# Optimization experiments

Measured on AMD Instinct MI355X. Metric: run time of the kernel, lower is better.

Reference implementation:

```python
import jax, jax.numpy as jnp
import numpy as np

N_NODES = 1_000_000
N_EDGES = 32_000_000
EPS_INIT = 100.0


def setup_inputs() -> dict:
    key = jax.random.key(0)
    ks = jax.random.split(key, 8)
    x = jax.random.normal(ks[0], (N_NODES, 1), dtype=jnp.float32)
    edge_index = jax.random.randint(ks[1], (2, N_EDGES), 0, N_NODES, dtype=jnp.int64)
    # MLP params: Linear(1,20) -> ReLU -> Linear(20,20) -> ReLU -> Linear(20,1)
    w1 = jax.random.normal(ks[2], (1, 20), dtype=jnp.float32) / np.sqrt(1.0)
    b1 = jnp.zeros((20,), dtype=jnp.float32)
    w2 = jax.random.normal(ks[3], (20, 20), dtype=jnp.float32) / np.sqrt(20.0)
    b2 = jnp.zeros((20,), dtype=jnp.float32)
    w3 = jax.random.normal(ks[4], (20, 1), dtype=jnp.float32) / np.sqrt(20.0)
    b3 = jnp.zeros((1,), dtype=jnp.float32)
    eps = jnp.asarray(EPS_INIT, dtype=jnp.float32)
    return {"x": x, "edge_index": edge_index, "eps": eps,
            "w1": w1, "b1": b1, "w2": w2, "b2": b2, "w3": w3, "b3": b3}


def reference(x, edge_index, eps, w1, b1, w2, b2, w3, b3):
    # GINConv: out = MLP((1 + eps) * x + sum_{j in N(i)} x_j)
    src, dst = edge_index[0], edge_index[1]
    # gather source features per edge, scatter-add to destination nodes
    agg = jax.ops.segment_sum(x[src], dst, num_segments=N_NODES)  # [N, 1]
    h = (1.0 + eps) * x + agg
    h = jax.nn.relu(h @ w1 + b1)   # [N, 20]
    h = jax.nn.relu(h @ w2 + b2)   # [N, 20]
    out = h @ w3 + b3              # [N, 1]
    return out
```

## Files before the change

### kernel.cpp

```cpp
#include <hip/hip_runtime.h>

#define N_NODES 1000000
#define N_EDGES 32000000

#define NB        256
#define TSC       1024
#define EPB       125000
#define QPB       31250
#define NBKT      245
#define BKT_PAD   256
#define CAP       135168
#define RING      96

#define BINS_ELEMS  ((size_t)NBKT * CAP)
#define CNT_ELEMS   ((size_t)NB * BKT_PAD)
#define WS_NEEDED   ((BINS_ELEMS + CNT_ELEMS + BKT_PAD) * 4)

__global__ __launch_bounds__(TSC) void gin_count(const int* __restrict__ dst,
                                                 unsigned* __restrict__ cnt) {
    __shared__ unsigned h[BKT_PAD];
    int tid = threadIdx.x;
    if (tid < BKT_PAD) h[tid] = 0u;
    __syncthreads();
    int k = blockIdx.x;
    const int4* q = reinterpret_cast<const int4*>(dst) + (size_t)k * QPB;
    for (int i = tid; i < QPB; i += TSC) {
        int4 d = q[i];
        atomicAdd(&h[d.x >> 12], 1u);
        atomicAdd(&h[d.y >> 12], 1u);
        atomicAdd(&h[d.z >> 12], 1u);
        atomicAdd(&h[d.w >> 12], 1u);
    }
    __syncthreads();
    if (tid < BKT_PAD) cnt[(size_t)k * BKT_PAD + tid] = h[tid];
}

__global__ void gin_scan(unsigned* __restrict__ cnt, unsigned* __restrict__ tot) {
    int gtid = blockIdx.x * blockDim.x + threadIdx.x;
    int b = gtid >> 6;
    int lane = gtid & 63;
    if (b >= BKT_PAD) return;
    unsigned running = 0;
    for (int base = 0; base < NB; base += 64) {
        int idx = base + lane;
        unsigned v = (idx < NB) ? cnt[(size_t)idx * BKT_PAD + b] : 0u;
        unsigned s = v;
        for (int d = 1; d < 64; d <<= 1) {
            unsigned u = __shfl_up(s, d);
            if (lane >= d) s += u;
        }
        unsigned excl = s - v;
        if (idx < NB) cnt[(size_t)idx * BKT_PAD + b] = running + excl;
        running += __shfl(s, 63);
    }
    if (lane == 0) tot[b] = running;
}

__global__ __launch_bounds__(TSC) void gin_scatter_bins(const int* __restrict__ src,
                                                        const int* __restrict__ dst,
                                                        const unsigned* __restrict__ cnt,
                                                        unsigned* __restrict__ bins) {
    __shared__ unsigned stage[BKT_PAD][RING];
    __shared__ unsigned stot[BKT_PAD];
    __shared__ unsigned sflt[BKT_PAD];
    __shared__ unsigned sbase[BKT_PAD];

    int tid = threadIdx.x;
    int k = blockIdx.x;
    if (tid < BKT_PAD) {
        stot[tid] = 0u;
        sflt[tid] = 0u;
        sbase[tid] = cnt[(size_t)k * BKT_PAD + tid];
    }
    __syncthreads();

    const int4* qs = reinterpret_cast<const int4*>(src) + (size_t)k * QPB;
    const int4* qd = reinterpret_cast<const int4*>(dst) + (size_t)k * QPB;

    for (int t0 = 0; t0 < QPB; t0 += TSC) {
        int i = t0 + tid;
        if (i < QPB) {
            int4 s4 = qs[i];
            int4 d4 = qd[i];
#define PUT(ss, dd) do {                                                     \
            unsigned b_ = (unsigned)(dd) >> 12;                              \
            unsigned p_ = atomicAdd(&stot[b_], 1u);                          \
            stage[b_][p_ % RING] =                                           \
                (((unsigned)(dd) & 4095u) << 20) | (unsigned)(ss);           \
        } while (0)
            PUT(s4.x, d4.x);
            PUT(s4.y, d4.y);
            PUT(s4.z, d4.z);
            PUT(s4.w, d4.w);
#undef PUT
        }
        __syncthreads();
        if (tid < BKT_PAD) {
            unsigned b = (unsigned)tid;
            unsigned T = stot[b];
            unsigned F = sflt[b];
            if (F + 32 <= T) {
                unsigned gbase = sbase[b];
                unsigned* gout = bins + (size_t)b * CAP;
                while (F + 32 <= T) {
                    unsigned r = F % RING;
                    unsigned gp = gbase + F;
                    if (gp + 32 <= CAP) {
#pragma unroll
                        for (int c = 0; c < 32; ++c) gout[gp + c] = stage[b][r + c];
                    }
                    F += 32;
                }
                sflt[b] = F;
            }
        }
        __syncthreads();
    }
    if (tid < BKT_PAD) {
        unsigned b = (unsigned)tid;
        unsigned T = stot[b];
        unsigned F = sflt[b];
        unsigned gbase = sbase[b];
        unsigned* gout = bins + (size_t)b * CAP;
        for (; F < T; ++F) {
            unsigned gp = gbase + F;
            if (gp < CAP) gout[gp] = stage[b][F % RING];
        }
    }
}

__global__ __launch_bounds__(1024) void gin_reduce_mlp(const unsigned* __restrict__ bins,
                               const unsigned* __restrict__ tot,
                               const float* __restrict__ x,
                               const float* __restrict__ eps,
                               const float* __restrict__ w1,
                               const float* __restrict__ b1,
                               const float* __restrict__ w2,
                               const float* __restrict__ b2,
                               const float* __restrict__ w3,
                               const float* __restrict__ b3,
                               float* __restrict__ out) {
    __shared__ float acc[4096];
    int tid = threadIdx.x;
    int b = blockIdx.x;
    for (int i = tid; i < 4096; i += 1024) acc[i] = 0.0f;
    __syncthreads();

    unsigned n = tot[b];
    if (n > CAP) n = CAP;
    const unsigned* bb = bins + (size_t)b * CAP;
    const uint4* bb4 = reinterpret_cast<const uint4*>(bb);
    unsigned nq = n >> 2;
    for (unsigned i = tid; i < nq; i += 1024) {
        uint4 e = bb4[i];
        atomicAdd(&acc[e.x >> 20], x[e.x & 0xFFFFFu]);
        atomicAdd(&acc[e.y >> 20], x[e.y & 0xFFFFFu]);
        atomicAdd(&acc[e.z >> 20], x[e.z & 0xFFFFFu]);
        atomicAdd(&acc[e.w >> 20], x[e.w & 0xFFFFFu]);
    }
    for (unsigned i = (nq << 2) + tid; i < n; i += 1024) {
        unsigned e = bb[i];
        atomicAdd(&acc[e >> 20], x[e & 0xFFFFFu]);
    }
    __syncthreads();

    float epsv = 1.0f + eps[0];
    for (int j = tid; j < 4096; j += 1024) {
        int node = (b << 12) + j;
        if (node >= N_NODES) break;
        float h0 = epsv * x[node] + acc[j];

        float h1[20];
#pragma unroll
        for (int jj = 0; jj < 20; ++jj)
            h1[jj] = fmaxf(fmaf(h0, w1[jj], b1[jj]), 0.0f);

        float o = b3[0];
#pragma unroll
        for (int kk = 0; kk < 20; ++kk) {
            float a = b2[kk];
#pragma unroll
            for (int jj = 0; jj < 20; ++jj)
                a = fmaf(h1[jj], w2[jj * 20 + kk], a);
            o = fmaf(fmaxf(a, 0.0f), w3[kk], o);
        }
        out[node] = o;
    }
}

__global__ void gin_zero_kernel(float* __restrict__ agg, int n) {
    int i = blockIdx.x * blockDim.x + threadIdx.x;
    if (i < n) agg[i] = 0.0f;
}

__global__ void gin_scatter_kernel(const float* __restrict__ x,
                                   const int* __restrict__ src,
                                   const int* __restrict__ dst,
                                   float* __restrict__ agg) {
    int q = blockIdx.x * blockDim.x + threadIdx.x;
    int e = q * 4;
    if (e + 3 < N_EDGES) {
        int4 s = *reinterpret_cast<const int4*>(src + e);
        int4 d = *reinterpret_cast<const int4*>(dst + e);
        atomicAdd(&agg[d.x], x[s.x]);
        atomicAdd(&agg[d.y], x[s.y]);
        atomicAdd(&agg[d.z], x[s.z]);
        atomicAdd(&agg[d.w], x[s.w]);
    } else if (e < N_EDGES) {
        for (; e < N_EDGES; ++e) atomicAdd(&agg[dst[e]], x[src[e]]);
    }
}

__global__ void gin_mlp_kernel(const float* __restrict__ x,
                               const float* __restrict__ agg,
                               const float* __restrict__ eps,
                               const float* __restrict__ w1,
                               const float* __restrict__ b1,
                               const float* __restrict__ w2,
                               const float* __restrict__ b2,
                               const float* __restrict__ w3,
                               const float* __restrict__ b3,
                               float* __restrict__ out) {
    int i = blockIdx.x * blockDim.x + threadIdx.x;
    if (i >= N_NODES) return;
    float h0 = (1.0f + eps[0]) * x[i] + agg[i];
    float h1[20];
#pragma unroll
    for (int j = 0; j < 20; ++j) h1[j] = fmaxf(fmaf(h0, w1[j], b1[j]), 0.0f);
    float o = b3[0];
#pragma unroll
    for (int k = 0; k < 20; ++k) {
        float a = b2[k];
#pragma unroll
        for (int j = 0; j < 20; ++j) a = fmaf(h1[j], w2[j * 20 + k], a);
        o = fmaf(fmaxf(a, 0.0f), w3[k], o);
    }
    out[i] = o;
}

extern "C" void kernel_launch(void* const* d_in, const int* in_sizes, int n_in,
                              void* d_out, int out_size, void* d_ws, size_t ws_size,
                              hipStream_t stream) {
    const float* x    = (const float*)d_in[0];
    const int*   ei   = (const int*)  d_in[1];
    const float* eps  = (const float*)d_in[2];
    const float* w1   = (const float*)d_in[3];
    const float* b1   = (const float*)d_in[4];
    const float* w2   = (const float*)d_in[5];
    const float* b2   = (const float*)d_in[6];
    const float* w3   = (const float*)d_in[7];
    const float* b3   = (const float*)d_in[8];
    float* out = (float*)d_out;

    const int* src = ei;
    const int* dst = ei + N_EDGES;

    if (ws_size >= WS_NEEDED) {
        unsigned* bins = (unsigned*)d_ws;
        unsigned* cnt  = bins + BINS_ELEMS;
        unsigned* tot  = cnt + CNT_ELEMS;

        gin_count<<<NB, TSC, 0, stream>>>(dst, cnt);
        {
            int blocks = (BKT_PAD * 64 + 255) / 256;
            gin_scan<<<blocks, 256, 0, stream>>>(cnt, tot);
        }
        gin_scatter_bins<<<NB, TSC, 0, stream>>>(src, dst, cnt, bins);
        gin_reduce_mlp<<<NBKT, 1024, 0, stream>>>(bins, tot, x, eps,
                                                  w1, b1, w2, b2, w3, b3, out);
    } else {
        float* agg = (ws_size >= (size_t)N_NODES * sizeof(float)) ? (float*)d_ws : out;
        {
            int blocks = (N_NODES + 255) / 256;
            gin_zero_kernel<<<blocks, 256, 0, stream>>>(agg, N_NODES);
        }
        {
            int quads = N_EDGES / 4;
            int blocks = (quads + 255) / 256;
            gin_scatter_kernel<<<blocks, 256, 0, stream>>>(x, src, dst, agg);
        }
        {
            int blocks = (N_NODES + 255) / 256;
            gin_mlp_kernel<<<blocks, 256, 0, stream>>>(x, agg, eps, w1, b1, w2, b2,
                                                       w3, b3, out);
        }
    }
}
```

Before: 410.5 us.

## Split bucket reduction across two blocks and move MLP to separate combine kernel

The fused reduce+MLP kernel, launched with only 245 blocks, is split in two. The reduce kernel now uses two blocks per bucket, each handling half the binned edges and writing partial sums to a new workspace region. A separate kernel with one thread per node adds the two partials and runs the MLP. This doubles the grid for the gather/atomic phase to fill more CUs, at the cost of an extra launch, a larger workspace requirement, and extra global writes and reads of the partial sums.

```diff
diff --git a/kernel.cpp b/kernel.cpp
--- a/kernel.cpp
+++ b/kernel.cpp
@@ -14,7 +14,8 @@
 
 #define BINS_ELEMS  ((size_t)NBKT * CAP)
 #define CNT_ELEMS   ((size_t)NB * BKT_PAD)
-#define WS_NEEDED   ((BINS_ELEMS + CNT_ELEMS + BKT_PAD) * 4)
+#define PAGG_ELEMS  ((size_t)NBKT * 2 * 4096)
+#define WS_NEEDED   ((BINS_ELEMS + CNT_ELEMS + BKT_PAD + PAGG_ELEMS) * 4)
 
 __global__ __launch_bounds__(TSC) void gin_count(const int* __restrict__ dst,
                                                  unsigned* __restrict__ cnt) {
@@ -129,8 +130,45 @@
     }
 }
 
-__global__ __launch_bounds__(1024) void gin_reduce_mlp(const unsigned* __restrict__ bins,
-                               const unsigned* __restrict__ tot,
+__global__ __launch_bounds__(1024) void gin_reduce(const unsigned* __restrict__ bins,
+                                                   const unsigned* __restrict__ tot,
+                                                   const float* __restrict__ x,
+                                                   float* __restrict__ pagg) {
+    __shared__ float acc[4096];
+    int tid = threadIdx.x;
+    int blk = blockIdx.x;
+    int b = blk >> 1;
+    int h = blk & 1;
+    for (int i = tid; i < 4096; i += 1024) acc[i] = 0.0f;
+    __syncthreads();
+
+    unsigned n = tot[b];
+    if (n > CAP) n = CAP;
+    const unsigned* bb = bins + (size_t)b * CAP;
+    const uint4* bb4 = reinterpret_cast<const uint4*>(bb);
+    unsigned nq = n >> 2;
+    unsigned q_lo = h ? (nq >> 1) : 0;
+    unsigned q_hi = h ? nq : (nq >> 1);
+    for (unsigned i = q_lo + tid; i < q_hi; i += 1024) {
+        uint4 e = bb4[i];
+        atomicAdd(&acc[e.x >> 20], x[e.x & 0xFFFFFu]);
+        atomicAdd(&acc[e.y >> 20], x[e.y & 0xFFFFFu]);
+        atomicAdd(&acc[e.z >> 20], x[e.z & 0xFFFFFu]);
+        atomicAdd(&acc[e.w >> 20], x[e.w & 0xFFFFFu]);
+    }
+    if (h) {
+        for (unsigned i = (nq << 2) + tid; i < n; i += 1024) {
+            unsigned e = bb[i];
+            atomicAdd(&acc[e >> 20], x[e & 0xFFFFFu]);
+        }
+    }
+    __syncthreads();
+
+    float* po = pagg + (size_t)blk * 4096;
+    for (int i = tid; i < 4096; i += 1024) po[i] = acc[i];
+}
+
+__global__ __launch_bounds__(512) void gin_combine_mlp(const float* __restrict__ pagg,
                                const float* __restrict__ x,
                                const float* __restrict__ eps,
                                const float* __restrict__ w1,
@@ -140,52 +178,28 @@
                                const float* __restrict__ w3,
                                const float* __restrict__ b3,
                                float* __restrict__ out) {
-    __shared__ float acc[4096];
-    int tid = threadIdx.x;
-    int b = blockIdx.x;
-    for (int i = tid; i < 4096; i += 1024) acc[i] = 0.0f;
-    __syncthreads();
-
-    unsigned n = tot[b];
-    if (n > CAP) n = CAP;
-    const unsigned* bb = bins + (size_t)b * CAP;
-    const uint4* bb4 = reinterpret_cast<const uint4*>(bb);
-    unsigned nq = n >> 2;
-    for (unsigned i = tid; i < nq; i += 1024) {
-        uint4 e = bb4[i];
-        atomicAdd(&acc[e.x >> 20], x[e.x & 0xFFFFFu]);
-        atomicAdd(&acc[e.y >> 20], x[e.y & 0xFFFFFu]);
-        atomicAdd(&acc[e.z >> 20], x[e.z & 0xFFFFFu]);
-        atomicAdd(&acc[e.w >> 20], x[e.w & 0xFFFFFu]);
-    }
-    for (unsigned i = (nq << 2) + tid; i < n; i += 1024) {
-        unsigned e = bb[i];
-        atomicAdd(&acc[e >> 20], x[e & 0xFFFFFu]);
-    }
-    __syncthreads();
-
-    float epsv = 1.0f + eps[0];
-    for (int j = tid; j < 4096; j += 1024) {
-        int node = (b << 12) + j;
-        if (node >= N_NODES) break;
-        float h0 = epsv * x[node] + acc[j];
-
-        float h1[20];
+    int i = blockIdx.x * blockDim.x + threadIdx.x;
+    if (i >= N_NODES) return;
+    int b = i >> 12;
+    int j = i & 4095;
+    float agg = pagg[(size_t)(b * 2) * 4096 + j] + pagg[(size_t)(b * 2 + 1) * 4096 + j];
+    float h0 = (1.0f + eps[0]) * x[i] + agg;
+
+    float h1[20];
+#pragma unroll
+    for (int jj = 0; jj < 20; ++jj)
+        h1[jj] = fmaxf(fmaf(h0, w1[jj], b1[jj]), 0.0f);
+
+    float o = b3[0];
+#pragma unroll
+    for (int kk = 0; kk < 20; ++kk) {
+        float a = b2[kk];
 #pragma unroll
         for (int jj = 0; jj < 20; ++jj)
-            h1[jj] = fmaxf(fmaf(h0, w1[jj], b1[jj]), 0.0f);
-
-        float o = b3[0];
-#pragma unroll
-        for (int kk = 0; kk < 20; ++kk) {
-            float a = b2[kk];
-#pragma unroll
-            for (int jj = 0; jj < 20; ++jj)
-                a = fmaf(h1[jj], w2[jj * 20 + kk], a);
-            o = fmaf(fmaxf(a, 0.0f), w3[kk], o);
-        }
-        out[node] = o;
-    }
+            a = fmaf(h1[jj], w2[jj * 20 + kk], a);
+        o = fmaf(fmaxf(a, 0.0f), w3[kk], o);
+    }
+    out[i] = o;
 }
 
 __global__ void gin_zero_kernel(float* __restrict__ agg, int n) {
@@ -259,6 +273,7 @@
         unsigned* bins = (unsigned*)d_ws;
         unsigned* cnt  = bins + BINS_ELEMS;
         unsigned* tot  = cnt + CNT_ELEMS;
+        float*    pagg = (float*)(tot + BKT_PAD);
 
         gin_count<<<NB, TSC, 0, stream>>>(dst, cnt);
         {
@@ -266,8 +281,9 @@
             gin_scan<<<blocks, 256, 0, stream>>>(cnt, tot);
         }
         gin_scatter_bins<<<NB, TSC, 0, stream>>>(src, dst, cnt, bins);
-        gin_reduce_mlp<<<NBKT, 1024, 0, stream>>>(bins, tot, x, eps,
-                                                  w1, b1, w2, b2, w3, b3, out);
+        gin_reduce<<<NBKT * 2, 1024, 0, stream>>>(bins, tot, x, pagg);
+        gin_combine_mlp<<<(N_NODES + 511) / 512, 512, 0, stream>>>(pagg, x, eps,
+                                                 w1, b1, w2, b2, w3, b3, out);
     } else {
         float* agg = (ws_size >= (size_t)N_NODES * sizeof(float)) ? (float*)d_ws : out;
         {
```

New measurement: 408.6 us. No clear change (-0.5%).
